# Kernel tuning notes

Measured on AMD Instinct MI355X. Metric: run time of the kernel, lower is better.

## Reference

```python
import jax, jax.numpy as jnp
import numpy as np

B, S, D = 2, 2048, 2048
H, DH = 16, 128          # n_heads, head_dim
HFF = 8192               # hidden_dim (SwiGLU)
EPS = 1e-5               # layer_norm_eps passed to AdvancedRMSNorm


def setup_inputs() -> dict:
    key = jax.random.key(0)
    ks = jax.random.split(key, 16)
    sd = lambda fan_in: 1.0 / np.sqrt(fan_in)
    inp = {
        "x": jax.random.normal(ks[0], (B, S, D), jnp.float32),
        # attention (torch Linear weights: [out, in])
        "q_w": jax.random.normal(ks[1], (D, D), jnp.float32) * sd(D),
        "k_w": jax.random.normal(ks[2], (D, D), jnp.float32) * sd(D),
        "v_w": jax.random.normal(ks[3], (D, D), jnp.float32) * sd(D),
        "o_w": jax.random.normal(ks[4], (D, D), jnp.float32) * sd(D),
        "temp": jnp.ones((H, 1, 1), jnp.float32),  # learnable per-head temperature
        # RMSNorm scales
        "ln1_w": jnp.ones((D,), jnp.float32),
        "ln2_w": jnp.ones((D,), jnp.float32),
        # SwiGLU
        "gate_w": jax.random.normal(ks[5], (HFF, D), jnp.float32) * sd(D),
        "up_w": jax.random.normal(ks[6], (HFF, D), jnp.float32) * sd(D),
        "gate2_w": jax.random.normal(ks[7], (HFF, D), jnp.float32) * sd(D),
        "down_w": jax.random.normal(ks[8], (D, HFF), jnp.float32) * sd(HFF),
        # gated residual connections (Linear with bias)
        "ag_w": jax.random.normal(ks[9], (D, D), jnp.float32) * sd(D),
        "ag_b": jnp.zeros((D,), jnp.float32),
        "fg_w": jax.random.normal(ks[10], (D, D), jnp.float32) * sd(D),
        "fg_b": jnp.zeros((D,), jnp.float32),
    }
    return inp


def _rmsnorm(x, w):
    rms = jnp.sqrt(jnp.mean(x * x, axis=-1, keepdims=True) + EPS)
    return w * (x / rms)


def _l2norm(x):
    # F.normalize(dim=-1): x / max(||x||_2, 1e-12)
    n = jnp.sqrt(jnp.sum(x * x, axis=-1, keepdims=True))
    return x / jnp.maximum(n, 1e-12)


def _block(x, q_w, k_w, v_w, o_w, temp, ln1_w, ln2_w,
           gate_w, up_w, gate2_w, down_w, ag_w, ag_b, fg_w, fg_b):
    # --- cosine-sim attention sublayer ---
    residual = x
    h = _rmsnorm(x, ln1_w)
    q = (h @ q_w.T).reshape(B, S, H, DH).transpose(0, 2, 1, 3)  # [B,H,S,DH]
    k = (h @ k_w.T).reshape(B, S, H, DH).transpose(0, 2, 1, 3)
    v = (h @ v_w.T).reshape(B, S, H, DH).transpose(0, 2, 1, 3)
    q = _l2norm(q)
    k = _l2norm(k)
    scores = jnp.einsum("bhqd,bhkd->bhqk", q, k) * temp  # temp [H,1,1] broadcasts
    causal = jnp.triu(jnp.ones((S, S), bool), k=1)
    scores = jnp.where(causal, -jnp.inf, scores)
    attn = jax.nn.softmax(scores, axis=-1)
    out = jnp.einsum("bhqk,bhkd->bhqd", attn, v)
    out = out.transpose(0, 2, 1, 3).reshape(B, S, D)
    attn_out = out @ o_w.T
    # gated residual: sigmoid(W a + b)*a + (1-g)*residual
    g = jax.nn.sigmoid(attn_out @ ag_w.T + ag_b)
    x = g * attn_out + (1.0 - g) * residual
    # --- SwiGLU sublayer ---
    residual = x
    h = _rmsnorm(x, ln2_w)
    gate = jax.nn.silu(h @ gate_w.T)
    up = h @ up_w.T
    gate2 = jax.nn.sigmoid(h @ gate2_w.T)
    ffn_out = (gate * up * gate2) @ down_w.T
    g = jax.nn.sigmoid(ffn_out @ fg_w.T + fg_b)
    return g * ffn_out + (1.0 - g) * residual


def reference(x, q_w, k_w, v_w, o_w, temp, ln1_w, ln2_w,
              gate_w, up_w, gate2_w, down_w, ag_w, ag_b, fg_w, fg_b):
    return _block(x, q_w, k_w, v_w, o_w, temp, ln1_w, ln2_w,
                  gate_w, up_w, gate2_w, down_w, ag_w, ag_b, fg_w, fg_b)
```

## Files before the change

kernel.cpp:

```cpp
#include <hip/hip_runtime.h>

typedef unsigned short u16;
typedef unsigned int u32;
using bf16x8 = __attribute__((ext_vector_type(8))) short;
using f32x4  = __attribute__((ext_vector_type(4))) float;

#define EPS 1e-5f

__device__ __forceinline__ u16 f2bf(float f) {
    union { float f; u32 u; } v; v.f = f;
    u32 r = v.u + 0x7FFFu + ((v.u >> 16) & 1u);
    return (u16)(r >> 16);
}
__device__ __forceinline__ float bf2f(u16 u) {
    union { u32 u; float f; } v; v.u = ((u32)u) << 16;
    return v.f;
}
__device__ __forceinline__ void gl16(const void* g, void* s) {
    __builtin_amdgcn_global_load_lds(
        (const __attribute__((address_space(1))) u32*)g,
        (__attribute__((address_space(3))) u32*)s, 16, 0, 0);
}
__device__ __forceinline__ float sigm(float x) { return 1.f / (1.f + __expf(-x)); }

__global__ void conv_bf16(const float* __restrict__ src, u16* __restrict__ dst, int n4) {
    int i = blockIdx.x * 256 + threadIdx.x;
    if (i >= n4) return;
    float4 v = reinterpret_cast<const float4*>(src)[i];
    u32 lo = (u32)f2bf(v.x) | ((u32)f2bf(v.y) << 16);
    u32 hi = (u32)f2bf(v.z) | ((u32)f2bf(v.w) << 16);
    reinterpret_cast<uint2*>(dst)[i] = make_uint2(lo, hi);
}

__global__ void conv3_bf16(const float* __restrict__ s0, const float* __restrict__ s1,
                           const float* __restrict__ s2, u16* __restrict__ d0,
                           u16* __restrict__ d1, u16* __restrict__ d2, int n4) {
    int i = blockIdx.x * 256 + threadIdx.x;
    if (i >= n4) return;
    const float* src = (blockIdx.y == 0) ? s0 : (blockIdx.y == 1) ? s1 : s2;
    u16* dst = (blockIdx.y == 0) ? d0 : (blockIdx.y == 1) ? d1 : d2;
    float4 v = reinterpret_cast<const float4*>(src)[i];
    u32 lo = (u32)f2bf(v.x) | ((u32)f2bf(v.y) << 16);
    u32 hi = (u32)f2bf(v.z) | ((u32)f2bf(v.w) << 16);
    reinterpret_cast<uint2*>(dst)[i] = make_uint2(lo, hi);
}

__global__ void rmsnorm_k(const float* __restrict__ x, const float* __restrict__ wt,
                          u16* __restrict__ out) {
    __shared__ float red[4];
    const int row = blockIdx.x, t = threadIdx.x;
    const float* xr = x + (size_t)row * 2048;
    float4 v0 = *reinterpret_cast<const float4*>(&xr[t * 8]);
    float4 v1 = *reinterpret_cast<const float4*>(&xr[t * 8 + 4]);
    float ss = v0.x*v0.x + v0.y*v0.y + v0.z*v0.z + v0.w*v0.w
             + v1.x*v1.x + v1.y*v1.y + v1.z*v1.z + v1.w*v1.w;
#pragma unroll
    for (int d = 1; d < 64; d <<= 1) ss += __shfl_xor(ss, d);
    if ((t & 63) == 0) red[t >> 6] = ss;
    __syncthreads();
    const float tot = red[0] + red[1] + red[2] + red[3];
    const float s = 1.f / sqrtf(tot * (1.f / 2048.f) + EPS);
    float4 w0 = *reinterpret_cast<const float4*>(&wt[t * 8]);
    float4 w1 = *reinterpret_cast<const float4*>(&wt[t * 8 + 4]);
    u32 o[4];
    o[0] = (u32)f2bf(v0.x * s * w0.x) | ((u32)f2bf(v0.y * s * w0.y) << 16);
    o[1] = (u32)f2bf(v0.z * s * w0.z) | ((u32)f2bf(v0.w * s * w0.w) << 16);
    o[2] = (u32)f2bf(v1.x * s * w1.x) | ((u32)f2bf(v1.y * s * w1.y) << 16);
    o[3] = (u32)f2bf(v1.z * s * w1.z) | ((u32)f2bf(v1.w * s * w1.w) << 16);
    *reinterpret_cast<uint4*>(&out[(size_t)row * 2048 + t * 8]) =
        make_uint4(o[0], o[1], o[2], o[3]);
}

__global__ void qk_l2norm(u16* __restrict__ qkv, const float* __restrict__ temp) {
    const int wid = blockIdx.x * 4 + (threadIdx.x >> 6);
    const int l = threadIdx.x & 63;
    const int n = wid >> 5;
    const int rem = wid & 31;
    const int which = rem >> 4;
    const int h = rem & 15;
    u16* p = qkv + (size_t)n * 6144 + which * 2048 + h * 128 + l * 2;
    u32 v = *reinterpret_cast<const u32*>(p);
    float f0 = bf2f((u16)(v & 0xffff)), f1 = bf2f((u16)(v >> 16));
    float ss = f0 * f0 + f1 * f1;
#pragma unroll
    for (int d = 1; d < 64; d <<= 1) ss += __shfl_xor(ss, d);
    float sc = 1.f / fmaxf(sqrtf(ss), 1e-12f);
    if (which == 0) sc *= temp[h];
    *reinterpret_cast<u32*>(p) = (u32)f2bf(f0 * sc) | ((u32)f2bf(f1 * sc) << 16);
}

__global__ __launch_bounds__(512, 1)
void gemm_big(const u16* __restrict__ A, const u16* __restrict__ B,
              u16* __restrict__ outB, int M, int N, int K, int ldc) {
    extern __shared__ u16 lds[];
    const int nbn = N >> 8;
    const int nwg = (M >> 8) * nbn;
    const int orig = blockIdx.x;
    const int q8 = nwg >> 3, r8 = nwg & 7;
    const int xcd = orig & 7, lin = orig >> 3;
    const int wgid = (xcd < r8 ? xcd * (q8 + 1) : r8 * (q8 + 1) + (xcd - r8) * q8) + lin;
    const int g = wgid / (nbn << 2);
    const int rem = wgid - g * (nbn << 2);
    const int bn = rem >> 2;
    const int bm = (g << 2) + (rem & 3);

    const int t = threadIdx.x;
    const int w = t >> 6, l = t & 63;
    const int lr = l & 15, lg = l >> 4;
    const int NT = K >> 6;

    const int srow = t >> 3;
    const int scg  = (t & 7) ^ (srow & 7);
    const u16* aS0 = A + (size_t)(bm * 256 + srow) * K + scg * 8;
    const u16* aS1 = aS0 + (size_t)128 * K;
    const u16* bS0 = B + (size_t)(bn * 256 + srow) * K + scg * 8;
    const u16* bS1 = bS0 + (size_t)128 * K;
    const size_t r64 = (size_t)64 * K;

#define STG(slot, src, ko) do {                                     \
        gl16((src) + (ko), (slot) + t * 8);                         \
        gl16((src) + (ko) + r64, (slot) + 4096 + t * 8);            \
    } while (0)

    f32x4 acc[16][2];
#pragma unroll
    for (int i = 0; i < 16; i++) { acc[i][0] = (f32x4){0,0,0,0}; acc[i][1] = (f32x4){0,0,0,0}; }

    const int xr = (lr & 7) << 4;
    const int kof[2] = { ((lg) << 4) ^ xr, ((4 + lg) << 4) ^ xr };

    STG(lds + 16384, bS0, 0);
    STG(lds + 24576, bS1, 0);
    STG(lds + 0,     aS0, 0);
    STG(lds + 8192,  aS1, 0);
    asm volatile("s_waitcnt vmcnt(2)" ::: "memory");
    __builtin_amdgcn_s_barrier();

    for (int T = 0; T < NT; ++T) {
        const char* rb = (const char*)lds + (size_t)(T & 1) * 65536;
        u16* sb = lds + ((T + 1) & 1) * 32768;
        const bool st = (T + 1) < NT;
        const size_t ko = (size_t)(T + 1) * 64;
        bf16x8 bfr[2][2];
#pragma unroll
        for (int p = 0; p < 4; ++p) {
            bf16x8 af[4][2];
#pragma unroll
            for (int m2 = 0; m2 < 4; m2++) {
                const int hrow = (p & 1) * 64 + m2 * 16 + lr;
                const char* ab = rb + (p >> 1) * 16384 + hrow * 128;
                af[m2][0] = *reinterpret_cast<const bf16x8*>(ab + kof[0]);
                af[m2][1] = *reinterpret_cast<const bf16x8*>(ab + kof[1]);
            }
            if (p == 0) {
#pragma unroll
                for (int n = 0; n < 2; n++) {
                    const int hrow = (w & 3) * 32 + n * 16 + lr;
                    const char* bb = rb + 32768 + (w >> 2) * 16384 + hrow * 128;
                    bfr[n][0] = *reinterpret_cast<const bf16x8*>(bb + kof[0]);
                    bfr[n][1] = *reinterpret_cast<const bf16x8*>(bb + kof[1]);
                }
            }
            if (st) {
                if (p == 0) STG(sb + 16384, bS0, ko);
                if (p == 1) STG(sb + 24576, bS1, ko);
                if (p == 2) STG(sb + 0,     aS0, ko);
                if (p == 3) STG(sb + 8192,  aS1, ko);
            }
            __builtin_amdgcn_s_barrier();
            __builtin_amdgcn_s_setprio(1);
#pragma unroll
            for (int m2 = 0; m2 < 4; m2++)
#pragma unroll
                for (int n = 0; n < 2; n++) {
                    acc[p * 4 + m2][n] = __builtin_amdgcn_mfma_f32_16x16x32_bf16(
                        af[m2][0], bfr[n][0], acc[p * 4 + m2][n], 0, 0, 0);
                    acc[p * 4 + m2][n] = __builtin_amdgcn_mfma_f32_16x16x32_bf16(
                        af[m2][1], bfr[n][1], acc[p * 4 + m2][n], 0, 0, 0);
                }
            __builtin_amdgcn_s_setprio(0);
            if (p == 1) {
                if (st) asm volatile("s_waitcnt vmcnt(4)" ::: "memory");
                else    asm volatile("s_waitcnt vmcnt(0)" ::: "memory");
            }
            if (p == 3 && st) asm volatile("s_waitcnt vmcnt(2)" ::: "memory");
            __builtin_amdgcn_s_barrier();
        }
    }
#undef STG

#pragma unroll
    for (int m = 0; m < 16; m++) {
        const int row = bm * 256 + m * 16 + lg * 4;
#pragma unroll
        for (int n = 0; n < 2; n++) {
            const int col = bn * 256 + w * 32 + n * 16 + lr;
#pragma unroll
            for (int q = 0; q < 4; q++)
                outB[(size_t)(row + q) * ldc + col] = f2bf(acc[m][n][q]);
        }
    }
}

template <int EPI>
__global__ __launch_bounds__(512, 1)
void gemm_bt(const u16* __restrict__ A, const u16* __restrict__ B,
             float* __restrict__ outF, u16* __restrict__ outB,
             const float* __restrict__ bias, const float* __restrict__ addend,
             const float* __restrict__ resid, float* __restrict__ outG,
             int M, int N, int K, int ldc) {
    extern __shared__ u16 lds[];
    const int nbn = N >> 8;
    const int nwg = (M >> 7) * nbn;
    const int orig = blockIdx.x;
    const int q8 = nwg >> 3, r8 = nwg & 7;
    const int xcd = orig & 7, lin = orig >> 3;
    const int wgid = (xcd < r8 ? xcd * (q8 + 1) : r8 * (q8 + 1) + (xcd - r8) * q8) + lin;
    const int g = wgid / (nbn << 3);
    const int rem = wgid - g * (nbn << 3);
    const int bn = rem >> 3;
    const int bm = (g << 3) + (rem & 7);

    const int t = threadIdx.x;
    const int w = t >> 6, l = t & 63;
    const int wr = w >> 2, wc = w & 3;
    const int lr = l & 15, lg = l >> 4;
    const int NT = K >> 6;

    const int pr = t >> 3, ps = t & 7;
    const int sg = ps ^ (pr & 7);
    const u16* aSrc = A + (size_t)(bm * 128 + pr) * K + sg * 8;
    const u16* bSrc = B + (size_t)(bn * 256 + pr) * K + sg * 8;
    const size_t rowStep = (size_t)64 * K;

#define STAGE_P0(TT, bi) do {                                                   \
        u16* da = lds + (bi) * 24576 + t * 8;                                   \
        gl16(aSrc + (size_t)(TT) * 64, da);                                     \
        gl16(aSrc + rowStep + (size_t)(TT) * 64, da + 4096);                    \
        gl16(bSrc + (size_t)(TT) * 64, lds + (bi) * 24576 + 8192 + t * 8);      \
    } while (0)
#define STAGE_P1(TT, bi) do {                                                   \
        u16* db = lds + (bi) * 24576 + 8192 + t * 8;                            \
        gl16(bSrc + rowStep + (size_t)(TT) * 64, db + 4096);                    \
        gl16(bSrc + 2 * rowStep + (size_t)(TT) * 64, db + 8192);                \
        gl16(bSrc + 3 * rowStep + (size_t)(TT) * 64, db + 12288);               \
    } while (0)

    f32x4 acc[4][4];
#pragma unroll
    for (int i = 0; i < 4; i++)
#pragma unroll
        for (int j = 0; j < 4; j++) acc[i][j] = (f32x4){0.f, 0.f, 0.f, 0.f};

    const int xr = (lr & 7) << 4;
    const int kof0 = ((lg) << 4) ^ xr;
    const int kof1 = ((4 + lg) << 4) ^ xr;

    STAGE_P0(0, 0); STAGE_P1(0, 0);
    if (NT > 1) {
        STAGE_P0(1, 1); STAGE_P1(1, 1);
        asm volatile("s_waitcnt vmcnt(6)" ::: "memory");
    } else {
        asm volatile("s_waitcnt vmcnt(0)" ::: "memory");
    }
    __builtin_amdgcn_s_barrier();

    for (int T = 0; T < NT; ++T) {
        const int bi = T % 3;
        const int sbi = (T + 2) % 3;
        const bool st = (T + 2) < NT;
        const char* bufA = (const char*)(lds + bi * 24576);
        const char* bufB = bufA + 16384;
        bf16x8 bf[4][2], af[2][2];
#pragma unroll
        for (int n = 0; n < 4; n++) {
            const int rb = wc * 64 + n * 16 + lr;
            bf[n][0] = *reinterpret_cast<const bf16x8*>(bufB + rb * 128 + kof0);
            bf[n][1] = *reinterpret_cast<const bf16x8*>(bufB + rb * 128 + kof1);
        }
#pragma unroll
        for (int m = 0; m < 2; m++) {
            const int ra = wr * 64 + m * 16 + lr;
            af[m][0] = *reinterpret_cast<const bf16x8*>(bufA + ra * 128 + kof0);
            af[m][1] = *reinterpret_cast<const bf16x8*>(bufA + ra * 128 + kof1);
        }
        if (st) STAGE_P0(T + 2, sbi);
        __builtin_amdgcn_s_barrier();
        __builtin_amdgcn_s_setprio(1);
#pragma unroll
        for (int m = 0; m < 2; m++)
#pragma unroll
            for (int n = 0; n < 4; n++) {
                acc[m][n] = __builtin_amdgcn_mfma_f32_16x16x32_bf16(af[m][0], bf[n][0], acc[m][n], 0, 0, 0);
                acc[m][n] = __builtin_amdgcn_mfma_f32_16x16x32_bf16(af[m][1], bf[n][1], acc[m][n], 0, 0, 0);
            }
        __builtin_amdgcn_s_setprio(0);
        __builtin_amdgcn_s_barrier();
        bf16x8 ag[2][2];
#pragma unroll
        for (int m = 0; m < 2; m++) {
            const int ra = wr * 64 + (m + 2) * 16 + lr;
            ag[m][0] = *reinterpret_cast<const bf16x8*>(bufA + ra * 128 + kof0);
            ag[m][1] = *reinterpret_cast<const bf16x8*>(bufA + ra * 128 + kof1);
        }
        if (st) STAGE_P1(T + 2, sbi);
        __builtin_amdgcn_s_barrier();
        __builtin_amdgcn_s_setprio(1);
#pragma unroll
        for (int m = 0; m < 2; m++)
#pragma unroll
            for (int n = 0; n < 4; n++) {
                acc[m + 2][n] = __builtin_amdgcn_mfma_f32_16x16x32_bf16(ag[m][0], bf[n][0], acc[m + 2][n], 0, 0, 0);
                acc[m + 2][n] = __builtin_amdgcn_mfma_f32_16x16x32_bf16(ag[m][1], bf[n][1], acc[m + 2][n], 0, 0, 0);
            }
        __builtin_amdgcn_s_setprio(0);
        if (st) {
            asm volatile("s_waitcnt vmcnt(6)" ::: "memory");
        } else if (T + 1 < NT) {
            asm volatile("s_waitcnt vmcnt(0)" ::: "memory");
        }
        __builtin_amdgcn_s_barrier();
    }
#undef STAGE_P0
#undef STAGE_P1

#pragma unroll
    for (int m = 0; m < 4; m++) {
        const int row = bm * 128 + wr * 64 + m * 16 + lg * 4;
#pragma unroll
        for (int n = 0; n < 4; n++) {
            const int col = bn * 256 + wc * 64 + n * 16 + lr;
#pragma unroll
            for (int q = 0; q < 4; q++) {
                const size_t idx = (size_t)(row + q) * ldc + col;
                const float v = acc[m][n][q];
                if (EPI == 0) {
                    outB[idx] = f2bf(v);
                } else if (EPI == 1) {
                    outF[idx] = v;
                    outB[idx] = f2bf(v);
                } else {
                    const float g2 = sigm(v + bias[col]);
                    outG[idx] = g2 * addend[idx] + (1.f - g2) * resid[idx];
                }
            }
        }
    }
}

#define VSWZ(dh) (((((dh) >> 3) ^ (dh)) & 7) << 4)
__global__ __launch_bounds__(512) void flash_attn(const u16* __restrict__ qkv,
                                                  u16* __restrict__ out) {
    __shared__ u16 klds[2][64 * 128];
    __shared__ u16 vlds[2][128 * 64];
    __shared__ u16 plds[8][16 * 64];
    const int t = threadIdx.x, w = t >> 6, l = t & 63;
    const int lr = l & 15, lg = l >> 4;
    const int b0 = blockIdx.x;
    const int xcd = b0 & 7, i0 = b0 >> 3;
    const int bh = ((i0 & 3) << 3) | xcd;
    const int p = i0 >> 2;
    const int b = bh >> 4, h = bh & 15;
    const size_t base = (size_t)b * 2048;
    const int sr0 = t >> 4;
    const int sc0 = (t & 15) << 3;

    uint4 kreg0, kreg1, vreg0, vreg1;

#define STAGE_LOAD(KT) do {                                                          \
        const size_t gg = (base + (size_t)(KT) * 64 + sr0) * 6144 + h * 128 + sc0;   \
        kreg0 = *reinterpret_cast<const uint4*>(&qkv[gg + 2048]);                    \
        vreg0 = *reinterpret_cast<const uint4*>(&qkv[gg + 4096]);                    \
        kreg1 = *reinterpret_cast<const uint4*>(&qkv[gg + 32 * 6144 + 2048]);        \
        vreg1 = *reinterpret_cast<const uint4*>(&qkv[gg + 32 * 6144 + 4096]);        \
    } while (0)

#define STAGE_WRITE(BUF) do {                                                                     \
        char* kb = (char*)&klds[BUF][0];                                                          \
        char* vb = (char*)&vlds[BUF][0];                                                          \
        *reinterpret_cast<uint4*>(kb + ((sr0 * 256 + sc0 * 2) ^ ((sr0 & 7) << 4))) = kreg0;       \
        *reinterpret_cast<uint4*>(kb + (((sr0 + 32) * 256 + sc0 * 2) ^ ((sr0 & 7) << 4))) = kreg1;\
        union { uint4 u; u16 s[8]; } vv;                                                          \
        vv.u = vreg0;                                                                             \
        _Pragma("unroll")                                                                         \
        for (int jj = 0; jj < 8; jj++) {                                                          \
            const int dh = sc0 + jj;                                                              \
            *reinterpret_cast<u16*>(vb + ((dh * 128 + sr0 * 2) ^ VSWZ(dh))) = vv.s[jj];           \
        }                                                                                         \
        vv.u = vreg1;                                                                             \
        _Pragma("unroll")                                                                         \
        for (int jj = 0; jj < 8; jj++) {                                                          \
            const int dh = sc0 + jj;                                                              \
            *reinterpret_cast<u16*>(vb + ((dh * 128 + (sr0 + 32) * 2) ^ VSWZ(dh))) = vv.s[jj];    \
        }                                                                                         \
    } while (0)

    for (int phase = 0; phase < 2; ++phase) {
        const int qt = phase ? (15 - p) : p;
        const int last = 2 * qt + 1;
        const int qrow = qt * 128 + w * 16 + lr;
        const int qr0 = qt * 128 + w * 16 + lg * 4;
        bf16x8 qf[4];
#pragma unroll
        for (int kk = 0; kk < 4; kk++)
            qf[kk] = *reinterpret_cast<const bf16x8*>(
                &qkv[(base + qrow) * 6144 + h * 128 + kk * 32 + lg * 8]);
        f32x4 o[8];
#pragma unroll
        for (int i = 0; i < 8; i++) o[i] = (f32x4){0.f, 0.f, 0.f, 0.f};
        float m[4] = {-1e30f, -1e30f, -1e30f, -1e30f};
        float ls[4] = {0.f, 0.f, 0.f, 0.f};

        STAGE_LOAD(0);
        int cur = 0;
        STAGE_WRITE(0);
        __syncthreads();

        for (int kt = 0; kt <= last; ++kt) {
            if (kt < last) STAGE_LOAD(kt + 1);
            const char* kb = (const char*)&klds[cur][0];
            const char* vb = (const char*)&vlds[cur][0];
            f32x4 s[4];
#pragma unroll
            for (int nf = 0; nf < 4; nf++) {
                f32x4 a = (f32x4){0.f, 0.f, 0.f, 0.f};
                const int kv = nf * 16 + lr;
#pragma unroll
                for (int kk = 0; kk < 4; kk++) {
                    bf16x8 kf = *reinterpret_cast<const bf16x8*>(
                        kb + ((kv * 256 + kk * 64 + lg * 16) ^ ((kv & 7) << 4)));
                    a = __builtin_amdgcn_mfma_f32_16x16x32_bf16(qf[kk], kf, a, 0, 0, 0);
                }
                s[nf] = a;
            }
            if (kt >= 2 * qt) {
#pragma unroll
                for (int nf = 0; nf < 4; nf++) {
                    const int kvi = kt * 64 + nf * 16 + lr;
#pragma unroll
                    for (int q = 0; q < 4; q++)
                        if (kvi > qr0 + q) s[nf][q] = -1e30f;
                }
            }
            float mx[4] = {-1e30f, -1e30f, -1e30f, -1e30f};
#pragma unroll
            for (int nf = 0; nf < 4; nf++)
#pragma unroll
                for (int q = 0; q < 4; q++) mx[q] = fmaxf(mx[q], s[nf][q]);
#pragma unroll
            for (int q = 0; q < 4; q++) {
#pragma unroll
                for (int d = 1; d < 16; d <<= 1) mx[q] = fmaxf(mx[q], __shfl_xor(mx[q], d));
            }
            float fac[4], rs[4];
#pragma unroll
            for (int q = 0; q < 4; q++) {
                const float mn = fmaxf(m[q], mx[q]);
                fac[q] = __expf(m[q] - mn);
                m[q] = mn;
                rs[q] = 0.f;
            }
#pragma unroll
            for (int nf = 0; nf < 4; nf++) {
#pragma unroll
                for (int q = 0; q < 4; q++) {
                    const float pv = __expf(s[nf][q] - m[q]);
                    s[nf][q] = pv;
                    rs[q] += pv;
                }
            }
#pragma unroll
            for (int nf = 0; nf < 4; nf++) {
                const int col = nf * 16 + lr;
#pragma unroll
                for (int q = 0; q < 4; q++) {
                    const int row = lg * 4 + q;
                    *reinterpret_cast<u16*>((char*)&plds[w][0] +
                        ((row * 128 + col * 2) ^ ((row & 7) << 4))) = f2bf(s[nf][q]);
                }
            }
#pragma unroll
            for (int q = 0; q < 4; q++) {
#pragma unroll
                for (int d = 1; d < 16; d <<= 1) rs[q] += __shfl_xor(rs[q], d);
                ls[q] = ls[q] * fac[q] + rs[q];
            }
#pragma unroll
            for (int nf2 = 0; nf2 < 8; nf2++)
#pragma unroll
                for (int q = 0; q < 4; q++) o[nf2][q] *= fac[q];
#pragma unroll
            for (int ks = 0; ks < 2; ks++) {
                bf16x8 pf = *reinterpret_cast<const bf16x8*>((char*)&plds[w][0] +
                    ((lr * 128 + ks * 64 + lg * 16) ^ ((lr & 7) << 4)));
#pragma unroll
                for (int nf2 = 0; nf2 < 8; nf2++) {
                    const int dh = nf2 * 16 + lr;
                    bf16x8 vf = *reinterpret_cast<const bf16x8*>(
                        vb + ((dh * 128 + ks * 64 + lg * 16) ^ VSWZ(dh)));
                    o[nf2] = __builtin_amdgcn_mfma_f32_16x16x32_bf16(pf, vf, o[nf2], 0, 0, 0);
                }
            }
            if (kt < last) STAGE_WRITE(cur ^ 1);
            __syncthreads();
            cur ^= 1;
        }
#pragma unroll
        for (int nf2 = 0; nf2 < 8; nf2++) {
            const int col = h * 128 + nf2 * 16 + lr;
#pragma unroll
            for (int q = 0; q < 4; q++) {
                const float v = o[nf2][q] / ls[q];
                out[(base + qr0 + q) * 2048 + col] = f2bf(v);
            }
        }
        __syncthreads();
    }
#undef STAGE_LOAD
#undef STAGE_WRITE
}

__global__ void swiglu_comb(const u16* __restrict__ f3, u16* __restrict__ comb) {
    const size_t u = (size_t)blockIdx.x * 256 + threadIdx.x;
    const size_t n = u >> 8;
    const int f = (int)(u & 255) << 3;
    const u16* gp = f3 + n * 6144 + f;
    union { uint4 q; u16 s[8]; } g, up, g2;
    g.q  = *reinterpret_cast<const uint4*>(gp);
    up.q = *reinterpret_cast<const uint4*>(gp + 2048);
    g2.q = *reinterpret_cast<const uint4*>(gp + 4096);
    u32 r[4];
#pragma unroll
    for (int i = 0; i < 4; i++) {
        float a0 = bf2f(g.s[2 * i]),     a1 = bf2f(g.s[2 * i + 1]);
        float b0 = bf2f(up.s[2 * i]),    b1 = bf2f(up.s[2 * i + 1]);
        float c0 = bf2f(g2.s[2 * i]),    c1 = bf2f(g2.s[2 * i + 1]);
        float r0 = a0 * sigm(a0) * b0 * sigm(c0);
        float r1 = a1 * sigm(a1) * b1 * sigm(c1);
        r[i] = (u32)f2bf(r0) | ((u32)f2bf(r1) << 16);
    }
    *reinterpret_cast<uint4*>(comb + n * 8192 + f) = make_uint4(r[0], r[1], r[2], r[3]);
}

extern "C" void kernel_launch(void* const* d_in, const int* in_sizes, int n_in,
                              void* d_out, int out_size, void* d_ws, size_t ws_size,
                              hipStream_t stream) {
    const float* x      = (const float*)d_in[0];
    const float* q_w    = (const float*)d_in[1];
    const float* k_w    = (const float*)d_in[2];
    const float* v_w    = (const float*)d_in[3];
    const float* o_w    = (const float*)d_in[4];
    const float* temp   = (const float*)d_in[5];
    const float* ln1_w  = (const float*)d_in[6];
    const float* ln2_w  = (const float*)d_in[7];
    const float* gate_w = (const float*)d_in[8];
    const float* up_w   = (const float*)d_in[9];
    const float* gate2_w= (const float*)d_in[10];
    const float* down_w = (const float*)d_in[11];
    const float* ag_w   = (const float*)d_in[12];
    const float* ag_b   = (const float*)d_in[13];
    const float* fg_w   = (const float*)d_in[14];
    const float* fg_b   = (const float*)d_in[15];

    const int GEMM_LDS = 147456;
    const int BIG_LDS  = 131072;
    (void)hipFuncSetAttribute(reinterpret_cast<const void*>(&gemm_bt<0>),
                              hipFuncAttributeMaxDynamicSharedMemorySize, GEMM_LDS);
    (void)hipFuncSetAttribute(reinterpret_cast<const void*>(&gemm_bt<1>),
                              hipFuncAttributeMaxDynamicSharedMemorySize, GEMM_LDS);
    (void)hipFuncSetAttribute(reinterpret_cast<const void*>(&gemm_bt<2>),
                              hipFuncAttributeMaxDynamicSharedMemorySize, GEMM_LDS);
    (void)hipFuncSetAttribute(reinterpret_cast<const void*>(&gemm_big),
                              hipFuncAttributeMaxDynamicSharedMemorySize, BIG_LDS);

    char* ws = (char*)d_ws;
    u16*  Wbuf = (u16*)(ws);
    u16*  hbuf = (u16*)(ws + 33554432);
    float* x1  = (float*)(ws + 50331648);
    u16*  combo= (u16*)(ws + 83886080);
    char* E    = ws + 150994944;
    char* F    = ws + 201326592;
    u16*  ffb  = (u16*)(ws + 234881024);

    u16*   qkvact = (u16*)E;
    float* aof    = (float*)E;
    u16*   aob    = (u16*)(E + 33554432);
    u16*   ffn3q  = (u16*)E;
    u16*   attnb  = (u16*)F;
    float* fff    = (float*)F;

    float* outp = (float*)d_out;
    const size_t DD = 2048ull * 2048ull;
    const int cg_d = (int)(DD / 4) / 256;
    const int GRID_BIG = 16 * 24;
    const int GRID_SM  = 32 * 8;

    hipLaunchKernelGGL(rmsnorm_k, dim3(4096), dim3(256), 0, stream, x, ln1_w, hbuf);

    hipLaunchKernelGGL(conv3_bf16, dim3(cg_d, 3), dim3(256), 0, stream,
                       q_w, k_w, v_w, Wbuf, Wbuf + DD, Wbuf + 2 * DD, (int)(DD / 4));
    hipLaunchKernelGGL(gemm_big, dim3(GRID_BIG), dim3(512), BIG_LDS, stream,
                       hbuf, Wbuf, qkvact, 4096, 6144, 2048, 6144);

    hipLaunchKernelGGL(qk_l2norm, dim3(32768), dim3(256), 0, stream, qkvact, temp);

    hipLaunchKernelGGL(flash_attn, dim3(256), dim3(512), 0, stream, qkvact, attnb);

    hipLaunchKernelGGL(conv_bf16, dim3(cg_d), dim3(256), 0, stream, o_w, Wbuf, (int)(DD / 4));
    hipLaunchKernelGGL((gemm_bt<1>), dim3(GRID_SM), dim3(512), GEMM_LDS, stream,
                       attnb, Wbuf, aof, aob,
                       (const float*)nullptr, (const float*)nullptr, (const float*)nullptr,
                       (float*)nullptr, 4096, 2048, 2048, 2048);

    hipLaunchKernelGGL(conv_bf16, dim3(cg_d), dim3(256), 0, stream, ag_w, Wbuf, (int)(DD / 4));
    hipLaunchKernelGGL((gemm_bt<2>), dim3(GRID_SM), dim3(512), GEMM_LDS, stream,
                       aob, Wbuf, (float*)nullptr, (u16*)nullptr,
                       ag_b, aof, x, x1, 4096, 2048, 2048, 2048);

    hipLaunchKernelGGL(rmsnorm_k, dim3(4096), dim3(256), 0, stream, x1, ln2_w, hbuf);

    for (int qd = 0; qd < 4; qd++) {
        const size_t wofs = (size_t)qd * 2048 * 2048;
        hipLaunchKernelGGL(conv3_bf16, dim3(cg_d, 3), dim3(256), 0, stream,
                           gate_w + wofs, up_w + wofs, gate2_w + wofs,
                           Wbuf, Wbuf + 2048 * 2048, Wbuf + 2ull * 2048 * 2048, (int)(DD / 4));
        hipLaunchKernelGGL(gemm_big, dim3(GRID_BIG), dim3(512), BIG_LDS, stream,
                           hbuf, Wbuf, ffn3q, 4096, 6144, 2048, 6144);
        hipLaunchKernelGGL(swiglu_comb, dim3(4096), dim3(256), 0, stream, ffn3q, combo + qd * 2048);
    }

    hipLaunchKernelGGL(conv_bf16, dim3(16384), dim3(256), 0, stream, down_w, Wbuf, (int)(2048ull * 8192 / 4));
    hipLaunchKernelGGL((gemm_bt<1>), dim3(GRID_SM), dim3(512), GEMM_LDS, stream,
                       combo, Wbuf, fff, ffb,
                       (const float*)nullptr, (const float*)nullptr, (const float*)nullptr,
                       (float*)nullptr, 4096, 2048, 8192, 2048);

    hipLaunchKernelGGL(conv_bf16, dim3(cg_d), dim3(256), 0, stream, fg_w, Wbuf, (int)(DD / 4));
    hipLaunchKernelGGL((gemm_bt<2>), dim3(GRID_SM), dim3(512), GEMM_LDS, stream,
                       ffb, Wbuf, (float*)nullptr, (u16*)nullptr,
                       fg_b, fff, x1, outp, 4096, 2048, 2048, 2048);
}
```

Measured before the change: 1.186 ms.

## Reshape gemm_big wave tiling to 2x4 and use one barrier per K-tile

Each wave in gemm_big now computes a 128x64 output sub-tile (2x4 wave grid) instead of a 256x32 strip. B fragments are loaded once per K-tile and reused across four M sub-blocks. A fragments are loaded per K-half, so each wave reads less from LDS for each MFMA. The per-phase barriers and staggered vmcnt waits are replaced by a single vmcnt(0) plus barrier at the end of each K-tile. That cuts synchronisation overhead but may expose more global-load latency, because the prefetch must fully land before the next tile starts.

```diff
diff --git a/kernel.cpp b/kernel.cpp
--- a/kernel.cpp
+++ b/kernel.cpp
@@ -106,6 +106,7 @@
 
     const int t = threadIdx.x;
     const int w = t >> 6, l = t & 63;
+    const int wr = w >> 2, wc = w & 3;
     const int lr = l & 15, lg = l >> 4;
     const int NT = K >> 6;
 
@@ -122,9 +123,11 @@
         gl16((src) + (ko) + r64, (slot) + 4096 + t * 8);            \
     } while (0)
 
-    f32x4 acc[16][2];
-#pragma unroll
-    for (int i = 0; i < 16; i++) { acc[i][0] = (f32x4){0,0,0,0}; acc[i][1] = (f32x4){0,0,0,0}; }
+    f32x4 acc[8][4];
+#pragma unroll
+    for (int i = 0; i < 8; i++)
+#pragma unroll
+        for (int j = 0; j < 4; j++) acc[i][j] = (f32x4){0.f, 0.f, 0.f, 0.f};
 
     const int xr = (lr & 7) << 4;
     const int kof[2] = { ((lg) << 4) ^ xr, ((4 + lg) << 4) ^ xr };
@@ -133,33 +136,31 @@
     STG(lds + 24576, bS1, 0);
     STG(lds + 0,     aS0, 0);
     STG(lds + 8192,  aS1, 0);
-    asm volatile("s_waitcnt vmcnt(2)" ::: "memory");
+    asm volatile("s_waitcnt vmcnt(0)" ::: "memory");
     __builtin_amdgcn_s_barrier();
 
     for (int T = 0; T < NT; ++T) {
-        const char* rb = (const char*)lds + (size_t)(T & 1) * 65536;
+        const char* base = (const char*)lds + (size_t)(T & 1) * 65536;
         u16* sb = lds + ((T + 1) & 1) * 32768;
         const bool st = (T + 1) < NT;
         const size_t ko = (size_t)(T + 1) * 64;
-        bf16x8 bfr[2][2];
+        const char* aB = base + wr * 16384;
+        const char* bB = base + 32768 + (wc >> 1) * 16384 + (wc & 1) * 8192;
+        bf16x8 bfr[4][2];
+#pragma unroll
+        for (int n = 0; n < 4; n++) {
+            const int rb = n * 16 + lr;
+            bfr[n][0] = *reinterpret_cast<const bf16x8*>(bB + rb * 128 + kof[0]);
+            bfr[n][1] = *reinterpret_cast<const bf16x8*>(bB + rb * 128 + kof[1]);
+        }
 #pragma unroll
         for (int p = 0; p < 4; ++p) {
-            bf16x8 af[4][2];
+            const int ks = p >> 1, mh = p & 1;
+            bf16x8 af[4];
 #pragma unroll
             for (int m2 = 0; m2 < 4; m2++) {
-                const int hrow = (p & 1) * 64 + m2 * 16 + lr;
-                const char* ab = rb + (p >> 1) * 16384 + hrow * 128;
-                af[m2][0] = *reinterpret_cast<const bf16x8*>(ab + kof[0]);
-                af[m2][1] = *reinterpret_cast<const bf16x8*>(ab + kof[1]);
-            }
-            if (p == 0) {
-#pragma unroll
-                for (int n = 0; n < 2; n++) {
-                    const int hrow = (w & 3) * 32 + n * 16 + lr;
-                    const char* bb = rb + 32768 + (w >> 2) * 16384 + hrow * 128;
-                    bfr[n][0] = *reinterpret_cast<const bf16x8*>(bb + kof[0]);
-                    bfr[n][1] = *reinterpret_cast<const bf16x8*>(bb + kof[1]);
-                }
+                const int ra = mh * 64 + m2 * 16 + lr;
+                af[m2] = *reinterpret_cast<const bf16x8*>(aB + ra * 128 + kof[ks]);
             }
             if (st) {
                 if (p == 0) STG(sb + 16384, bS0, ko);
@@ -167,34 +168,28 @@
                 if (p == 2) STG(sb + 0,     aS0, ko);
                 if (p == 3) STG(sb + 8192,  aS1, ko);
             }
+            __builtin_amdgcn_s_setprio(1);
+#pragma unroll
+            for (int m2 = 0; m2 < 4; m2++)
+#pragma unroll
+                for (int n = 0; n < 4; n++)
+                    acc[mh * 4 + m2][n] = __builtin_amdgcn_mfma_f32_16x16x32_bf16(
+                        af[m2], bfr[n][ks], acc[mh * 4 + m2][n], 0, 0, 0);
+            __builtin_amdgcn_s_setprio(0);
+        }
+        if (st) {
+            asm volatile("s_waitcnt vmcnt(0)" ::: "memory");
             __builtin_amdgcn_s_barrier();
-            __builtin_amdgcn_s_setprio(1);
-#pragma unroll
-            for (int m2 = 0; m2 < 4; m2++)
-#pragma unroll
-                for (int n = 0; n < 2; n++) {
-                    acc[p * 4 + m2][n] = __builtin_amdgcn_mfma_f32_16x16x32_bf16(
-                        af[m2][0], bfr[n][0], acc[p * 4 + m2][n], 0, 0, 0);
-                    acc[p * 4 + m2][n] = __builtin_amdgcn_mfma_f32_16x16x32_bf16(
-                        af[m2][1], bfr[n][1], acc[p * 4 + m2][n], 0, 0, 0);
-                }
-            __builtin_amdgcn_s_setprio(0);
-            if (p == 1) {
-                if (st) asm volatile("s_waitcnt vmcnt(4)" ::: "memory");
-                else    asm volatile("s_waitcnt vmcnt(0)" ::: "memory");
-            }
-            if (p == 3 && st) asm volatile("s_waitcnt vmcnt(2)" ::: "memory");
-            __builtin_amdgcn_s_barrier();
         }
     }
 #undef STG
 
 #pragma unroll
-    for (int m = 0; m < 16; m++) {
-        const int row = bm * 256 + m * 16 + lg * 4;
-#pragma unroll
-        for (int n = 0; n < 2; n++) {
-            const int col = bn * 256 + w * 32 + n * 16 + lr;
+    for (int m = 0; m < 8; m++) {
+        const int row = bm * 256 + wr * 128 + m * 16 + lg * 4;
+#pragma unroll
+        for (int n = 0; n < 4; n++) {
+            const int col = bn * 256 + wc * 64 + n * 16 + lr;
 #pragma unroll
             for (int q = 0; q < 4; q++)
                 outB[(size_t)(row + q) * ldc + col] = f2bf(acc[m][n][q]);
```

Result: faster. 1.113 ms (-6.2%).
